# Optimization experiments

Measured on AMD Instinct MI355X. Metric: run time of the kernel, lower is better.

## Reference

```python
import jax, jax.numpy as jnp
import numpy as np

N_STREAMS = 8
DIM = 1024
N_HEADS = 16
HEAD_DIM = DIM // N_HEADS
STREAM_DIM = DIM // N_STREAMS
EPS = 1e-6


def setup_inputs() -> dict:
    key = jax.random.key(0)
    ks = jax.random.split(key, 20)
    B, S, D = 2, 2048, DIM
    inp = {
        "x": jax.random.normal(ks[0], (B, S, D), jnp.float32),
        "rope_cos": jax.random.uniform(ks[1], (S, HEAD_DIM), jnp.float32),
        "rope_sin": jax.random.uniform(ks[2], (S, HEAD_DIM), jnp.float32),
        # DeltaOperator: learned per-channel decay logits
        "delta_decay": jax.random.normal(ks[3], (D,), jnp.float32) * 0.02,
        # gate_proj: Linear(D, 3*n)
        "gate_w": jax.random.normal(ks[4], (3 * N_STREAMS, D), jnp.float32) * 0.02,
        "gate_b": jnp.zeros((3 * N_STREAMS,), jnp.float32),
        "phi_res": jax.random.normal(ks[5], (N_STREAMS, N_STREAMS), jnp.float32) * 0.02,
        "ln1_w": jnp.ones((D,), jnp.float32),
        "ln2_w": jnp.ones((D,), jnp.float32),
        # MLP (StrategicLinear == Linear at inference)
        "w1": jax.random.normal(ks[6], (4 * D, D), jnp.float32) * 0.02,
        "b1": jnp.zeros((4 * D,), jnp.float32),
        "w2": jax.random.normal(ks[7], (D, 4 * D), jnp.float32) * 0.02,
        "b2": jnp.zeros((D,), jnp.float32),
        # nn.MultiheadAttention params
        "in_proj_w": jax.random.normal(ks[8], (3 * D, D), jnp.float32) * 0.02,
        "in_proj_b": jnp.zeros((3 * D,), jnp.float32),
        "out_w": jax.random.normal(ks[9], (D, D), jnp.float32) * 0.02,
        "out_b": jnp.zeros((D,), jnp.float32),
    }
    return inp


def delta_operator(x, decay_logits):
    # out_t = x_t - s_{t-1};  s_t = beta*s_{t-1} + (1-beta)*x_t  (per-channel EMA delta)
    beta = jax.nn.sigmoid(decay_logits)  # [D]

    def step(s, xt):
        out = xt - s
        s_new = beta * s + (1.0 - beta) * xt
        return s_new, out

    xT = jnp.swapaxes(x, 0, 1)  # [S,B,D]
    s0 = jnp.zeros_like(xT[0])
    _, ysT = jax.lax.scan(step, s0, xT)
    return jnp.swapaxes(ysT, 0, 1)  # [B,S,D]


def rms_norm(x, w):
    var = jnp.mean(x * x, axis=-1, keepdims=True)
    return x * jax.lax.rsqrt(var + EPS) * w


def sinkhorn_knopp(phi, iterations=15):
    K = jnp.exp(phi)
    for _ in range(iterations):
        K = K / jnp.sum(K, axis=1, keepdims=True)
        K = K / jnp.sum(K, axis=0, keepdims=True)
    return K


def causal_mha(x, in_proj_w, in_proj_b, out_w, out_b):
    B, S, D = x.shape
    qkv = x @ in_proj_w.T + in_proj_b  # [B,S,3D]
    q, k, v = jnp.split(qkv, 3, axis=-1)
    def heads(t):
        return t.reshape(B, S, N_HEADS, HEAD_DIM).transpose(0, 2, 1, 3)  # [B,H,S,hd]
    q, k, v = heads(q), heads(k), heads(v)
    scores = jnp.einsum("bhqd,bhkd->bhqk", q, k) / jnp.sqrt(jnp.float32(HEAD_DIM))
    mask = jnp.tril(jnp.ones((S, S), bool))
    scores = jnp.where(mask, scores, jnp.float32(-1e9))
    attn = jax.nn.softmax(scores, axis=-1)
    o = jnp.einsum("bhqk,bhkd->bhqd", attn, v)
    o = o.transpose(0, 2, 1, 3).reshape(B, S, D)
    return o @ out_w.T + out_b


def reference(x, rope_cos, rope_sin, delta_decay, gate_w, gate_b, phi_res,
              ln1_w, ln2_w, w1, b1, w2, b2, in_proj_w, in_proj_b, out_w, out_b):
    B, S, D = x.shape
    n = N_STREAMS
    x_delta = delta_operator(x, delta_decay)
    x_state = jnp.mean(x_delta, axis=1)  # [B,D]
    gates = x_state @ gate_w.T + gate_b  # [B,3n]
    g_res = jax.nn.sigmoid(gates[:, 2 * n:])[:, None, :, None]  # [B,1,n,1]
    H_res = sinkhorn_knopp(phi_res, 15)
    x_streams = x_delta.reshape(B, S, n, STREAM_DIM)
    # (x_perm @ H.T).permute back == einsum over stream axis
    mhc_out = jnp.einsum("bsnd,mn->bsmd", x_streams * g_res, H_res).reshape(B, S, D)
    normed = rms_norm(x_delta, ln1_w)
    attn_out = causal_mha(normed, in_proj_w, in_proj_b, out_w, out_b)
    normed2 = rms_norm(x_delta + attn_out, ln2_w)
    h = jax.nn.gelu(normed2 @ w1.T + b1, approximate=False)
    ffn_out = h @ w2.T + b2
    return x_delta + attn_out + ffn_out + mhc_out
```

## Files before the change

### kernel.cpp

```cpp
#include <hip/hip_runtime.h>
#include <hip/hip_bf16.h>
#include <math.h>

#define BB 2
#define SS 2048
#define DDIM 1024
#define NHEAD 16
#define NSTR 8
#define SDIMC 128
#define NCH 16
#define CLEN 128
#define EPSV 1e-6f

using bf16 = __hip_bfloat16;
typedef __attribute__((ext_vector_type(8))) __bf16 bf8;
typedef __attribute__((ext_vector_type(4))) __bf16 bf4v;
typedef __attribute__((ext_vector_type(4))) float f4;

__device__ __forceinline__ bf16 f2b(float v) { return __float2bfloat16(v); }
__device__ __forceinline__ bf8 ld8(const bf16* p) { return *(const bf8*)p; }
__device__ __forceinline__ f4 MFMA(bf8 a, bf8 b, f4 c) {
  return __builtin_amdgcn_mfma_f32_16x16x32_bf16(a, b, c, 0, 0, 0);
}
__device__ __forceinline__ float sigm(float x) { return 1.0f / (1.0f + expf(-x)); }
__device__ __forceinline__ float fexp2(float x) { return __builtin_amdgcn_exp2f(x); }

__device__ __forceinline__ float gelu_f(float v) {
  float x = v * 0.70710678118654752f;
  float ax = fabsf(x);
  float t = __builtin_amdgcn_rcpf(1.0f + 0.3275911f * ax);
  float p = ((((1.061405429f * t - 1.453152027f) * t + 1.421413741f) * t
              - 0.284496736f) * t + 0.254829592f) * t;
  float e = 1.0f - p * fexp2(-ax * ax * 1.4426950408889634f);
  e = copysignf(e, x);
  return 0.5f * v * (1.0f + e);
}

__device__ __forceinline__ void glds16(bf16* l, const bf16* g) {
  __builtin_amdgcn_global_load_lds(
      (const __attribute__((address_space(1))) unsigned int*)g,
      (__attribute__((address_space(3))) unsigned int*)l, 16, 0, 0);
}

__global__ __launch_bounds__(256) void cvt_all(const float* __restrict__ ipw,
                                               const float* __restrict__ ow,
                                               const float* __restrict__ w1,
                                               const float* __restrict__ w2,
                                               bf16* __restrict__ WIPW,
                                               bf16* __restrict__ WOW,
                                               bf16* __restrict__ W1B,
                                               bf16* __restrict__ W2B) {
  const int S1 = 3 * DDIM * DDIM, S2 = S1 + DDIM * DDIM,
            S3 = S2 + 4 * DDIM * DDIM;
  int i4 = (blockIdx.x * 256 + threadIdx.x) * 4;
  const float* src;
  bf16* dst;
  int off;
  if (i4 < S1)      { src = ipw; dst = WIPW; off = i4; }
  else if (i4 < S2) { src = ow;  dst = WOW;  off = i4 - S1; }
  else if (i4 < S3) { src = w1;  dst = W1B;  off = i4 - S2; }
  else              { src = w2;  dst = W2B;  off = i4 - S3; }
  float4 v = *(const float4*)(src + off);
  bf4v o;
  o[0] = (__bf16)v.x; o[1] = (__bf16)v.y; o[2] = (__bf16)v.z; o[3] = (__bf16)v.w;
  *(bf4v*)(dst + off) = o;
}

__global__ __launch_bounds__(256) void delta_passA(const float* __restrict__ x,
                                                   const float* __restrict__ decay,
                                                   float* __restrict__ SA) {
  int idx = blockIdx.x * 256 + threadIdx.x;
  int d = idx % DDIM;
  int c = (idx / DDIM) % NCH;
  int b = idx / (DDIM * NCH);
  float beta = sigm(decay[d]);
  float omb = 1.0f - beta;
  const float* xp = x + ((size_t)(b * SS + c * CLEN)) * DDIM + d;
  float s = 0.0f;
  for (int j = 0; j < CLEN; j++) {
    float xv = xp[(size_t)j * DDIM];
    s = beta * s + omb * xv;
  }
  SA[idx] = s;
}

__global__ __launch_bounds__(256) void delta_passB(const float* __restrict__ SA,
                                                   const float* __restrict__ decay,
                                                   float* __restrict__ SIN) {
  int idx = blockIdx.x * 256 + threadIdx.x;
  int d = idx % DDIM;
  int b = idx / DDIM;
  float beta = sigm(decay[d]);
  float p = beta;
  for (int i = 0; i < 7; i++) p *= p;
  float s = 0.0f;
  for (int c = 0; c < NCH; c++) {
    SIN[(b * NCH + c) * DDIM + d] = s;
    s = p * s + SA[(b * NCH + c) * DDIM + d];
  }
}

__global__ __launch_bounds__(256) void delta_passC(const float* __restrict__ x,
                                                   const float* __restrict__ decay,
                                                   const float* __restrict__ SIN,
                                                   float* __restrict__ XD,
                                                   float* __restrict__ SA) {
  int idx = blockIdx.x * 256 + threadIdx.x;
  int d = idx % DDIM;
  int c = (idx / DDIM) % NCH;
  int b = idx / (DDIM * NCH);
  float beta = sigm(decay[d]);
  float omb = 1.0f - beta;
  const float* xp = x + ((size_t)(b * SS + c * CLEN)) * DDIM + d;
  float* xdp = XD + ((size_t)(b * SS + c * CLEN)) * DDIM + d;
  float s = SIN[idx];
  float sum = 0.0f;
  for (int j = 0; j < CLEN; j++) {
    float xv = xp[(size_t)j * DDIM];
    float o = xv - s;
    xdp[(size_t)j * DDIM] = o;
    sum += o;
    s = beta * s + omb * xv;
  }
  SA[idx] = sum;
}

__global__ __launch_bounds__(1024) void gates_sinkhorn(const float* __restrict__ SA,
                                                       const float* __restrict__ gw,
                                                       const float* __restrict__ gb,
                                                       const float* __restrict__ phi,
                                                       float* __restrict__ gres,
                                                       float* __restrict__ hres) {
  int tid = threadIdx.x;
  int wave = tid >> 6, lane = tid & 63;
  int b = wave >> 3, j = wave & 7;
  float acc = 0.0f;
  for (int d = lane; d < DDIM; d += 64) {
    float xs = 0.0f;
    for (int c = 0; c < NCH; c++) xs += SA[(b * NCH + c) * DDIM + d];
    xs *= (1.0f / (float)SS);
    acc += xs * gw[(2 * NSTR + j) * DDIM + d];
  }
  for (int off = 32; off > 0; off >>= 1) acc += __shfl_down(acc, off);
  if (lane == 0) gres[b * NSTR + j] = sigm(acc + gb[2 * NSTR + j]);
  __syncthreads();
  if (tid == 0) {
    float Km[8][8];
    for (int i = 0; i < 8; i++)
      for (int jj = 0; jj < 8; jj++) Km[i][jj] = expf(phi[i * 8 + jj]);
    for (int it = 0; it < 15; it++) {
      for (int i = 0; i < 8; i++) {
        float rs = 0.0f;
        for (int jj = 0; jj < 8; jj++) rs += Km[i][jj];
        float inv = 1.0f / rs;
        for (int jj = 0; jj < 8; jj++) Km[i][jj] *= inv;
      }
      for (int jj = 0; jj < 8; jj++) {
        float cs = 0.0f;
        for (int i = 0; i < 8; i++) cs += Km[i][jj];
        float inv = 1.0f / cs;
        for (int i = 0; i < 8; i++) Km[i][jj] *= inv;
      }
    }
    for (int i = 0; i < 8; i++)
      for (int jj = 0; jj < 8; jj++) hres[i * 8 + jj] = Km[i][jj];
  }
}

__global__ __launch_bounds__(256) void rmsnorm_k(const float* __restrict__ in,
                                                 const float* __restrict__ w,
                                                 bf16* __restrict__ out) {
  int row = blockIdx.x;
  const float* r = in + (size_t)row * DDIM;
  int tid = threadIdx.x;
  float ss = 0.0f;
  for (int i = tid; i < DDIM; i += 256) {
    float v = r[i];
    ss += v * v;
  }
  for (int off = 32; off > 0; off >>= 1) ss += __shfl_down(ss, off);
  __shared__ float red[4];
  if ((tid & 63) == 0) red[tid >> 6] = ss;
  __syncthreads();
  float tot = red[0] + red[1] + red[2] + red[3];
  float sc = rsqrtf(tot / (float)DDIM + EPSV);
  bf16* o = out + (size_t)row * DDIM;
  for (int i = tid; i < DDIM; i += 256) o[i] = f2b(r[i] * sc * w[i]);
}

template <int ODT, int EPI>
__global__ __launch_bounds__(256) void gemm_lds(const bf16* __restrict__ A,
                                                const bf16* __restrict__ W,
                                                const float* __restrict__ bias,
                                                const float* __restrict__ res,
                                                void* __restrict__ outp,
                                                int M, int N, int K) {
  __shared__ bf16 As[2][128 * 32];
  __shared__ bf16 Bs[2][128 * 32];
  int tid = threadIdx.x;
  int lane = tid & 63, wv = tid >> 6;
  int ml = lane & 15, quad = lane >> 4;
  int wr = wv >> 1, wc = wv & 1;
  int m0 = blockIdx.x * 128, n0 = blockIdx.y * 128;
  const bf16* ga[2];
  const bf16* gb[2];
  int lofs[2];
#pragma unroll
  for (int it = 0; it < 2; it++) {
    int c = it * 256 + tid;
    int row = c >> 2, kc = (c & 3) * 8;
    ga[it] = A + (size_t)(m0 + row) * K + kc;
    gb[it] = W + (size_t)(n0 + row) * K + kc;
    lofs[it] = c * 8;
  }
#pragma unroll
  for (int it = 0; it < 2; it++) {
    glds16(&As[0][lofs[it]], ga[it]);
    glds16(&Bs[0][lofs[it]], gb[it]);
  }
  f4 acc[4][4] = {};
  int nk = K >> 5;
  int cur = 0;
  __syncthreads();
  for (int t = 0; t < nk; t++) {
    if (t + 1 < nk) {
      int ko = (t + 1) * 32;
#pragma unroll
      for (int it = 0; it < 2; it++) {
        glds16(&As[cur ^ 1][lofs[it]], ga[it] + ko);
        glds16(&Bs[cur ^ 1][lofs[it]], gb[it] + ko);
      }
    }
    bf8 af[4], bfr[4];
#pragma unroll
    for (int mi = 0; mi < 4; mi++)
      af[mi] = ld8(&As[cur][(wr * 64 + mi * 16 + ml) * 32 + quad * 8]);
#pragma unroll
    for (int ni = 0; ni < 4; ni++)
      bfr[ni] = ld8(&Bs[cur][(wc * 64 + ni * 16 + ml) * 32 + quad * 8]);
#pragma unroll
    for (int mi = 0; mi < 4; mi++)
#pragma unroll
      for (int ni = 0; ni < 4; ni++)
        acc[mi][ni] = MFMA(af[mi], bfr[ni], acc[mi][ni]);
    __syncthreads();
    cur ^= 1;
  }
#pragma unroll
  for (int mi = 0; mi < 4; mi++)
#pragma unroll
    for (int ni = 0; ni < 4; ni++)
#pragma unroll
      for (int r = 0; r < 4; r++) {
        int row = m0 + wr * 64 + mi * 16 + quad * 4 + r;
        int col = n0 + wc * 64 + ni * 16 + ml;
        size_t idx = (size_t)row * N + col;
        float v = acc[mi][ni][r] + bias[col];
        if (EPI == 1) v = gelu_f(v);
        if (EPI == 2) v += res[idx];
        if (ODT == 1) ((bf16*)outp)[idx] = f2b(v);
        else ((float*)outp)[idx] = v;
      }
}

__global__ __launch_bounds__(256) void gemm_part2(const bf16* __restrict__ A,
                                                  const bf16* __restrict__ W,
                                                  float* __restrict__ P0,
                                                  float* __restrict__ P1,
                                                  int M, int N, int KS, int LDK) {
  __shared__ bf16 As[2][128 * 32];
  __shared__ bf16 Bs[2][128 * 32];
  int tid = threadIdx.x;
  int lane = tid & 63, wv = tid >> 6;
  int ml = lane & 15, quad = lane >> 4;
  int wr = wv >> 1, wc = wv & 1;
  int m0 = blockIdx.x * 128, n0 = blockIdx.y * 128;
  const bf16* Ab = A + blockIdx.z * KS;
  const bf16* Wb = W + blockIdx.z * KS;
  float* P = blockIdx.z ? P1 : P0;
  const bf16* ga[2];
  const bf16* gb[2];
  int lofs[2];
#pragma unroll
  for (int it = 0; it < 2; it++) {
    int c = it * 256 + tid;
    int row = c >> 2, kc = (c & 3) * 8;
    ga[it] = Ab + (size_t)(m0 + row) * LDK + kc;
    gb[it] = Wb + (size_t)(n0 + row) * LDK + kc;
    lofs[it] = c * 8;
  }
#pragma unroll
  for (int it = 0; it < 2; it++) {
    glds16(&As[0][lofs[it]], ga[it]);
    glds16(&Bs[0][lofs[it]], gb[it]);
  }
  f4 acc[4][4] = {};
  int nk = KS >> 5;
  int cur = 0;
  __syncthreads();
  for (int t = 0; t < nk; t++) {
    if (t + 1 < nk) {
      int ko = (t + 1) * 32;
#pragma unroll
      for (int it = 0; it < 2; it++) {
        glds16(&As[cur ^ 1][lofs[it]], ga[it] + ko);
        glds16(&Bs[cur ^ 1][lofs[it]], gb[it] + ko);
      }
    }
    bf8 af[4], bfr[4];
#pragma unroll
    for (int mi = 0; mi < 4; mi++)
      af[mi] = ld8(&As[cur][(wr * 64 + mi * 16 + ml) * 32 + quad * 8]);
#pragma unroll
    for (int ni = 0; ni < 4; ni++)
      bfr[ni] = ld8(&Bs[cur][(wc * 64 + ni * 16 + ml) * 32 + quad * 8]);
#pragma unroll
    for (int mi = 0; mi < 4; mi++)
#pragma unroll
      for (int ni = 0; ni < 4; ni++)
        acc[mi][ni] = MFMA(af[mi], bfr[ni], acc[mi][ni]);
    __syncthreads();
    cur ^= 1;
  }
#pragma unroll
  for (int mi = 0; mi < 4; mi++)
#pragma unroll
    for (int ni = 0; ni < 4; ni++)
#pragma unroll
      for (int r = 0; r < 4; r++) {
        int row = m0 + wr * 64 + mi * 16 + quad * 4 + r;
        int col = n0 + wc * 64 + ni * 16 + ml;
        P[(size_t)row * N + col] = acc[mi][ni][r];
      }
}

template <int ODT, int EPI>
__global__ __launch_bounds__(256) void gemm_lds64(const bf16* __restrict__ A,
                                                  const bf16* __restrict__ W,
                                                  const float* __restrict__ bias,
                                                  const float* __restrict__ res,
                                                  void* __restrict__ outp,
                                                  int M, int N, int K) {
  __shared__ bf16 As[2][64 * 32];
  __shared__ bf16 Bs[2][128 * 32];
  int tid = threadIdx.x;
  int lane = tid & 63, wv = tid >> 6;
  int ml = lane & 15, quad = lane >> 4;
  int wr = wv & 1, wc = wv >> 1;
  int m0 = blockIdx.x * 64, n0 = blockIdx.y * 128;
  const bf16* gaA;
  const bf16* gb[2];
  int lofA, lofs[2];
  {
    int c = tid;
    int row = c >> 2, kc = (c & 3) * 8;
    gaA = A + (size_t)(m0 + row) * K + kc;
    lofA = c * 8;
  }
#pragma unroll
  for (int it = 0; it < 2; it++) {
    int c = it * 256 + tid;
    int row = c >> 2, kc = (c & 3) * 8;
    gb[it] = W + (size_t)(n0 + row) * K + kc;
    lofs[it] = c * 8;
  }
  glds16(&As[0][lofA], gaA);
#pragma unroll
  for (int it = 0; it < 2; it++) glds16(&Bs[0][lofs[it]], gb[it]);
  f4 acc[2][4] = {};
  int nk = K >> 5;
  int cur = 0;
  __syncthreads();
  for (int t = 0; t < nk; t++) {
    if (t + 1 < nk) {
      int ko = (t + 1) * 32;
      glds16(&As[cur ^ 1][lofA], gaA + ko);
#pragma unroll
      for (int it = 0; it < 2; it++) glds16(&Bs[cur ^ 1][lofs[it]], gb[it] + ko);
    }
    bf8 af[2], bfr[4];
#pragma unroll
    for (int mi = 0; mi < 2; mi++)
      af[mi] = ld8(&As[cur][(wr * 32 + mi * 16 + ml) * 32 + quad * 8]);
#pragma unroll
    for (int ni = 0; ni < 4; ni++)
      bfr[ni] = ld8(&Bs[cur][(wc * 64 + ni * 16 + ml) * 32 + quad * 8]);
#pragma unroll
    for (int mi = 0; mi < 2; mi++)
#pragma unroll
      for (int ni = 0; ni < 4; ni++)
        acc[mi][ni] = MFMA(af[mi], bfr[ni], acc[mi][ni]);
    __syncthreads();
    cur ^= 1;
  }
#pragma unroll
  for (int mi = 0; mi < 2; mi++)
#pragma unroll
    for (int ni = 0; ni < 4; ni++)
#pragma unroll
      for (int r = 0; r < 4; r++) {
        int row = m0 + wr * 32 + mi * 16 + quad * 4 + r;
        int col = n0 + wc * 64 + ni * 16 + ml;
        size_t idx = (size_t)row * N + col;
        float v = acc[mi][ni][r] + bias[col];
        if (EPI == 1) v = gelu_f(v);
        if (EPI == 2) v += res[idx];
        if (ODT == 1) ((bf16*)outp)[idx] = f2b(v);
        else ((float*)outp)[idx] = v;
      }
}

__global__ __launch_bounds__(256) void vtrans(const bf16* __restrict__ qkv,
                                              bf16* __restrict__ VT) {
  int bid = blockIdx.x;
  int st = bid % (SS / 64);
  int h = (bid / (SS / 64)) % NHEAD;
  int b = bid / ((SS / 64) * NHEAD);
  __shared__ bf16 tile[64][65];
  int s0 = st * 64;
  int tid = threadIdx.x;
  for (int it = 0; it < 16; it++) {
    int sl = it * 4 + (tid >> 6), dl = tid & 63;
    tile[sl][dl] = qkv[(size_t)(b * SS + s0 + sl) * (3 * DDIM) + 2 * DDIM + h * 64 + dl];
  }
  __syncthreads();
  for (int it = 0; it < 16; it++) {
    int dl = it * 4 + (tid >> 6), sl = tid & 63;
    VT[((size_t)(b * NHEAD + h) * 64 + dl) * SS + s0 + sl] = tile[sl][dl];
  }
}

__device__ __forceinline__ void phase_tile(int kt, int q0, int nkt,
                                           const bf8* qf, f4* oacc,
                                           float* m_r, float* l_r,
                                           const bf16* __restrict__ Ks,
                                           const bf16* __restrict__ Vs,
                                           bf16 (*pl)[72], int ml, int quad) {
  if (kt >= nkt) return;
  const float SC = 0.125f * 1.44269504089f;
  int k0 = kt * 64;
  f4 sacc[4] = {{0,0,0,0},{0,0,0,0},{0,0,0,0},{0,0,0,0}};
  __builtin_amdgcn_s_setprio(1);
#pragma unroll
  for (int kk = 0; kk < 2; kk++)
#pragma unroll
    for (int c = 0; c < 4; c++) {
      int chunk = ((c * 16 + ml) << 3) + ((kk * 4 + quad) ^ (ml & 7));
      bf8 kf = ld8(&Ks[chunk * 8]);
      sacc[c] = MFMA(qf[kk], kf, sacc[c]);
    }
  __builtin_amdgcn_s_setprio(0);
  float sv[4][4];
#pragma unroll
  for (int c = 0; c < 4; c++)
#pragma unroll
    for (int r = 0; r < 4; r++) sv[c][r] = sacc[c][r] * SC;
  if (kt == nkt - 1) {
#pragma unroll
    for (int c = 0; c < 4; c++)
#pragma unroll
      for (int r = 0; r < 4; r++) {
        int qi = q0 + quad * 4 + r;
        int kj = k0 + c * 16 + ml;
        if (kj > qi) sv[c][r] = -1e9f;
      }
  }
  float alpha[4];
#pragma unroll
  for (int r = 0; r < 4; r++) {
    float mx = fmaxf(fmaxf(sv[0][r], sv[1][r]), fmaxf(sv[2][r], sv[3][r]));
#pragma unroll
    for (int off = 1; off < 16; off <<= 1) mx = fmaxf(mx, __shfl_xor(mx, off));
    float mn = fmaxf(m_r[r], mx);
    float rs = 0.0f;
#pragma unroll
    for (int c = 0; c < 4; c++) {
      float p = fexp2(sv[c][r] - mn);
      sv[c][r] = p;
      rs += p;
    }
#pragma unroll
    for (int off = 1; off < 16; off <<= 1) rs += __shfl_xor(rs, off);
    alpha[r] = fexp2(m_r[r] - mn);
    l_r[r] = l_r[r] * alpha[r] + rs;
    m_r[r] = mn;
  }
#pragma unroll
  for (int c = 0; c < 4; c++)
#pragma unroll
    for (int r = 0; r < 4; r++) oacc[c][r] *= alpha[r];
#pragma unroll
  for (int c = 0; c < 4; c++)
#pragma unroll
    for (int r = 0; r < 4; r++)
      pl[quad * 4 + r][c * 16 + ml] = f2b(sv[c][r]);
  bf8 pf[2];
#pragma unroll
  for (int kk = 0; kk < 2; kk++) pf[kk] = ld8(&pl[ml][kk * 32 + quad * 8]);
  __builtin_amdgcn_s_setprio(1);
#pragma unroll
  for (int c = 0; c < 4; c++)
#pragma unroll
    for (int kk = 0; kk < 2; kk++) {
      int chunk = ((c * 16 + ml) << 3) + ((kk * 4 + quad) ^ (ml & 7));
      bf8 vf = ld8(&Vs[chunk * 8]);
      oacc[c] = MFMA(pf[kk], vf, oacc[c]);
    }
  __builtin_amdgcn_s_setprio(0);
}

__global__ __launch_bounds__(256) void flash_attn(const bf16* __restrict__ qkv,
                                                  const bf16* __restrict__ VT,
                                                  bf16* __restrict__ obuf) {
  int rb = blockIdx.x;
  int bid = (rb & 7) * 64 + (rb >> 3);
  int j = bid & 15;
  int blk = (j & 1) ? (15 - (j >> 1)) : (j >> 1);
  int h = (bid >> 4) & 15;
  int b = bid >> 8;
  int tid = threadIdx.x;
  int wv = tid >> 6, lane = tid & 63;
  int ml = lane & 15, quad = lane >> 4;
  int idx0 = blk * 4 + wv;
  int idx1 = 127 - idx0;
  int q0a = idx0 * 16, q0b = idx1 * 16;
  int nkt0 = blk + 1;
  int nkt1 = 32 - blk;
  int maxn = nkt1;

  __shared__ __align__(16) bf16 Ks[2][64 * 64];
  __shared__ __align__(16) bf16 Vs[2][64 * 64];
  __shared__ __align__(16) bf16 plds[4][16][72];
  bf16 (*pl)[72] = plds[wv];

  bf8 qfa[2], qfb[2];
#pragma unroll
  for (int kk = 0; kk < 2; kk++) {
    qfa[kk] = ld8(qkv + (size_t)(b * SS + q0a + ml) * (3 * DDIM) + h * 64 + kk * 32 + quad * 8);
    qfb[kk] = ld8(qkv + (size_t)(b * SS + q0b + ml) * (3 * DDIM) + h * 64 + kk * 32 + quad * 8);
  }
  f4 oacca[4] = {{0,0,0,0},{0,0,0,0},{0,0,0,0},{0,0,0,0}};
  f4 oaccb[4] = {{0,0,0,0},{0,0,0,0},{0,0,0,0},{0,0,0,0}};
  float ma[4], la[4], mb[4], lb[4];
#pragma unroll
  for (int r = 0; r < 4; r++) {
    ma[r] = -1e30f; la[r] = 0.0f;
    mb[r] = -1e30f; lb[r] = 0.0f;
  }

  const bf16* kglob = qkv + (size_t)b * SS * (3 * DDIM) + DDIM + h * 64;
  const bf16* vglob = VT + (size_t)(b * NHEAD + h) * 64 * SS;

#pragma unroll
  for (int it = 0; it < 2; it++) {
    int lam = it * 256 + tid;
    int row = lam >> 3;
    int ch = (lam & 7) ^ (row & 7);
    glds16(&Ks[0][lam * 8], kglob + (size_t)row * (3 * DDIM) + ch * 8);
    glds16(&Vs[0][lam * 8], vglob + (size_t)row * SS + ch * 8);
  }
  __syncthreads();
  int cur = 0;
  for (int kt = 0; kt < maxn; kt++) {
    if (kt + 1 < maxn) {
      int k0n = (kt + 1) * 64;
#pragma unroll
      for (int it = 0; it < 2; it++) {
        int lam = it * 256 + tid;
        int row = lam >> 3;
        int ch = (lam & 7) ^ (row & 7);
        glds16(&Ks[cur ^ 1][lam * 8], kglob + (size_t)(k0n + row) * (3 * DDIM) + ch * 8);
        glds16(&Vs[cur ^ 1][lam * 8], vglob + (size_t)row * SS + k0n + ch * 8);
      }
    }
    phase_tile(kt, q0a, nkt0, qfa, oacca, ma, la, Ks[cur], Vs[cur], pl, ml, quad);
    phase_tile(kt, q0b, nkt1, qfb, oaccb, mb, lb, Ks[cur], Vs[cur], pl, ml, quad);
    __syncthreads();
    cur ^= 1;
  }
#pragma unroll
  for (int c = 0; c < 4; c++)
#pragma unroll
    for (int r = 0; r < 4; r++) {
      int rowa = q0a + quad * 4 + r;
      int rowb = q0b + quad * 4 + r;
      obuf[(size_t)(b * SS + rowa) * DDIM + h * 64 + c * 16 + ml] =
          f2b(oacca[c][r] / la[r]);
      obuf[(size_t)(b * SS + rowb) * DDIM + h * 64 + c * 16 + ml] =
          f2b(oaccb[c][r] / lb[r]);
    }
}

__global__ __launch_bounds__(256) void final_k(const float* __restrict__ y,
                                               const float* __restrict__ P0,
                                               const float* __restrict__ P1,
                                               const float* __restrict__ bias,
                                               const float* __restrict__ xd,
                                               const float* __restrict__ hres,
                                               const float* __restrict__ gres,
                                               float* __restrict__ out) {
  int row = blockIdx.x;
  int b = row / SS;
  int tid = threadIdx.x;
  __shared__ float cf[8][8];
  if (tid < 64) cf[tid >> 3][tid & 7] = hres[tid] * gres[b * NSTR + (tid & 7)];
  __syncthreads();
  const float* yr = y + (size_t)row * DDIM;
  const float* p0 = P0 + (size_t)row * DDIM;
  const float* p1 = P1 + (size_t)row * DDIM;
  const float* xr = xd + (size_t)row * DDIM;
  float* o = out + (size_t)row * DDIM;
  for (int i = tid; i < DDIM; i += 256) {
    int m = i >> 7, dd = i & 127;
    float acc = yr[i] + p0[i] + p1[i] + bias[i];
#pragma unroll
    for (int n = 0; n < 8; n++) acc += cf[m][n] * xr[n * SDIMC + dd];
    o[i] = acc;
  }
}

extern "C" void kernel_launch(void* const* d_in, const int* in_sizes, int n_in,
                              void* d_out, int out_size, void* d_ws, size_t ws_size,
                              hipStream_t stream) {
  const float* x     = (const float*)d_in[0];
  const float* decay = (const float*)d_in[3];
  const float* gw    = (const float*)d_in[4];
  const float* gb    = (const float*)d_in[5];
  const float* phi   = (const float*)d_in[6];
  const float* ln1   = (const float*)d_in[7];
  const float* ln2   = (const float*)d_in[8];
  const float* w1    = (const float*)d_in[9];
  const float* b1    = (const float*)d_in[10];
  const float* w2    = (const float*)d_in[11];
  const float* b2    = (const float*)d_in[12];
  const float* ipw   = (const float*)d_in[13];
  const float* ipb   = (const float*)d_in[14];
  const float* ow    = (const float*)d_in[15];
  const float* obs   = (const float*)d_in[16];
  float* out = (float*)d_out;

  const size_t MB = 1048576ull;
  char* wsp = (char*)d_ws;
  float* SA   = (float*)(wsp);
  float* SIN  = (float*)(wsp + 131072ull);
  float* GRES = (float*)(wsp + 262144ull);
  float* HRES = (float*)(wsp + 262208ull);
  float* XD   = (float*)(wsp + 1 * MB);
  float* AO   = (float*)(wsp + 17 * MB);
  bf16*  NORM = (bf16*)(wsp + 33 * MB);
  bf16*  OB   = (bf16*)(wsp + 41 * MB);
  bf16*  QKV  = (bf16*)(wsp + 49 * MB);
  bf16*  VT   = (bf16*)(wsp + 73 * MB);
  bf16*  HB   = (bf16*)(wsp + 49 * MB);
  bf16*  WIPW = (bf16*)(wsp + 81 * MB);
  bf16*  WOW  = (bf16*)(wsp + 87 * MB);
  bf16*  W1B  = (bf16*)(wsp + 89 * MB);
  bf16*  W2B  = (bf16*)(wsp + 97 * MB);
  float* PK0  = (float*)(wsp + 33 * MB);
  float* PK1  = (float*)(wsp + 81 * MB);

  cvt_all<<<dim3(12 * DDIM * DDIM / 1024), dim3(256), 0, stream>>>(
      ipw, ow, w1, w2, WIPW, WOW, W1B, W2B);

  delta_passA<<<dim3(BB * NCH * DDIM / 256), dim3(256), 0, stream>>>(x, decay, SA);
  delta_passB<<<dim3(BB * DDIM / 256), dim3(256), 0, stream>>>(SA, decay, SIN);
  delta_passC<<<dim3(BB * NCH * DDIM / 256), dim3(256), 0, stream>>>(x, decay, SIN, XD, SA);
  gates_sinkhorn<<<dim3(1), dim3(1024), 0, stream>>>(SA, gw, gb, phi, GRES, HRES);
  rmsnorm_k<<<dim3(BB * SS), dim3(256), 0, stream>>>(XD, ln1, NORM);
  gemm_lds<1, 0><<<dim3(32, 24), dim3(256), 0, stream>>>(NORM, WIPW, ipb, nullptr,
                                                         QKV, BB * SS, 3 * DDIM, DDIM);
  vtrans<<<dim3(BB * NHEAD * (SS / 64)), dim3(256), 0, stream>>>(QKV, VT);
  flash_attn<<<dim3(BB * NHEAD * 16), dim3(256), 0, stream>>>(QKV, VT, OB);
  gemm_lds64<0, 2><<<dim3(64, 8), dim3(256), 0, stream>>>(OB, WOW, obs, XD,
                                                          AO, BB * SS, DDIM, DDIM);
  rmsnorm_k<<<dim3(BB * SS), dim3(256), 0, stream>>>(AO, ln2, NORM);
  gemm_lds<1, 1><<<dim3(32, 32), dim3(256), 0, stream>>>(NORM, W1B, b1, nullptr,
                                                         HB, BB * SS, 4 * DDIM, DDIM);
  gemm_part2<<<dim3(32, 8, 2), dim3(256), 0, stream>>>(HB, W2B, PK0, PK1,
                                                       BB * SS, DDIM, 2 * DDIM, 4 * DDIM);
  final_k<<<dim3(BB * SS), dim3(256), 0, stream>>>(AO, PK0, PK1, b2, XD,
                                                   HRES, GRES, out);
}
```

Measured before the change: 443.6 us.

## Share K/V register fragments across both query tiles and transpose QK scores

The flash attention loop now loads K and V fragments from LDS into registers once per key tile and reuses them for both the short and long query tiles, where before each tile reloaded them. The QK MFMA operands are swapped so each lane holds the scores for one query row. That lets the row max and row sum use two cross-lane shuffles instead of four per row, and lets P be written to LDS as packed 4-wide stores. Per-wave P staging is split into two buffers so the two tiles' softmax and PV phases can be interleaved, at the cost of more registers and LDS.

New measurement: 425.6 us. 4.0% less time.

```diff
diff --git a/kernel.cpp b/kernel.cpp
--- a/kernel.cpp
+++ b/kernel.cpp
@@ -430,82 +430,78 @@
   }
 }
 
-__device__ __forceinline__ void phase_tile(int kt, int q0, int nkt,
-                                           const bf8* qf, f4* oacc,
-                                           float* m_r, float* l_r,
-                                           const bf16* __restrict__ Ks,
-                                           const bf16* __restrict__ Vs,
-                                           bf16 (*pl)[72], int ml, int quad) {
-  if (kt >= nkt) return;
+__device__ __forceinline__ void qk_softmax(bool active, int kt, int q0, int nkt,
+                                           const bf8 kf[4][2], const bf8* qf,
+                                           f4* oacc, float& m, float& l,
+                                           bf8* pf, bf16 (*pl)[72],
+                                           int ml, int quad, int k0) {
+  if (!active) return;
   const float SC = 0.125f * 1.44269504089f;
-  int k0 = kt * 64;
-  f4 sacc[4] = {{0,0,0,0},{0,0,0,0},{0,0,0,0},{0,0,0,0}};
+  f4 s[4] = {{0,0,0,0},{0,0,0,0},{0,0,0,0},{0,0,0,0}};
   __builtin_amdgcn_s_setprio(1);
 #pragma unroll
   for (int kk = 0; kk < 2; kk++)
 #pragma unroll
-    for (int c = 0; c < 4; c++) {
-      int chunk = ((c * 16 + ml) << 3) + ((kk * 4 + quad) ^ (ml & 7));
-      bf8 kf = ld8(&Ks[chunk * 8]);
-      sacc[c] = MFMA(qf[kk], kf, sacc[c]);
+    for (int c = 0; c < 4; c++)
+      s[c] = MFMA(kf[c][kk], qf[kk], s[c]);
+  __builtin_amdgcn_s_setprio(0);
+  if (kt == nkt - 1) {
+    int qi = q0 + ml;
+#pragma unroll
+    for (int c = 0; c < 4; c++)
+#pragma unroll
+      for (int r = 0; r < 4; r++)
+        if (k0 + c * 16 + quad * 4 + r > qi) s[c][r] = -1e30f;
+  }
+  float mx = s[0][0];
+#pragma unroll
+  for (int c = 0; c < 4; c++)
+#pragma unroll
+    for (int r = 0; r < 4; r++) mx = fmaxf(mx, s[c][r]);
+  mx = fmaxf(mx, __shfl_xor(mx, 16));
+  mx = fmaxf(mx, __shfl_xor(mx, 32));
+  float mn = fmaxf(m, mx * SC);
+  float alpha = fexp2(m - mn);
+  float rs = 0.0f;
+  float p[4][4];
+#pragma unroll
+  for (int c = 0; c < 4; c++)
+#pragma unroll
+    for (int r = 0; r < 4; r++) {
+      p[c][r] = fexp2(__builtin_fmaf(s[c][r], SC, -mn));
+      rs += p[c][r];
     }
-  __builtin_amdgcn_s_setprio(0);
-  float sv[4][4];
+  rs += __shfl_xor(rs, 16);
+  rs += __shfl_xor(rs, 32);
+  l = l * alpha + rs;
+  m = mn;
+  float alr[4];
+#pragma unroll
+  for (int r = 0; r < 4; r++) alr[r] = __shfl(alpha, quad * 4 + r);
 #pragma unroll
   for (int c = 0; c < 4; c++)
 #pragma unroll
-    for (int r = 0; r < 4; r++) sv[c][r] = sacc[c][r] * SC;
-  if (kt == nkt - 1) {
-#pragma unroll
-    for (int c = 0; c < 4; c++)
-#pragma unroll
-      for (int r = 0; r < 4; r++) {
-        int qi = q0 + quad * 4 + r;
-        int kj = k0 + c * 16 + ml;
-        if (kj > qi) sv[c][r] = -1e9f;
-      }
-  }
-  float alpha[4];
-#pragma unroll
-  for (int r = 0; r < 4; r++) {
-    float mx = fmaxf(fmaxf(sv[0][r], sv[1][r]), fmaxf(sv[2][r], sv[3][r]));
-#pragma unroll
-    for (int off = 1; off < 16; off <<= 1) mx = fmaxf(mx, __shfl_xor(mx, off));
-    float mn = fmaxf(m_r[r], mx);
-    float rs = 0.0f;
-#pragma unroll
-    for (int c = 0; c < 4; c++) {
-      float p = fexp2(sv[c][r] - mn);
-      sv[c][r] = p;
-      rs += p;
-    }
-#pragma unroll
-    for (int off = 1; off < 16; off <<= 1) rs += __shfl_xor(rs, off);
-    alpha[r] = fexp2(m_r[r] - mn);
-    l_r[r] = l_r[r] * alpha[r] + rs;
-    m_r[r] = mn;
-  }
+    for (int r = 0; r < 4; r++) oacc[c][r] *= alr[r];
+#pragma unroll
+  for (int c = 0; c < 4; c++) {
+    bf4v w;
+#pragma unroll
+    for (int r = 0; r < 4; r++) w[r] = (__bf16)p[c][r];
+    *(bf4v*)&pl[ml][c * 16 + quad * 4] = w;
+  }
+#pragma unroll
+  for (int kk = 0; kk < 2; kk++) pf[kk] = ld8(&pl[ml][kk * 32 + quad * 8]);
+}
+
+__device__ __forceinline__ void pv_acc(bool active, const bf8* pf,
+                                       const bf8 vf[4][2], f4* oacc) {
+  if (!active) return;
+  __builtin_amdgcn_s_setprio(1);
 #pragma unroll
   for (int c = 0; c < 4; c++)
 #pragma unroll
-    for (int r = 0; r < 4; r++) oacc[c][r] *= alpha[r];
-#pragma unroll
-  for (int c = 0; c < 4; c++)
-#pragma unroll
-    for (int r = 0; r < 4; r++)
-      pl[quad * 4 + r][c * 16 + ml] = f2b(sv[c][r]);
-  bf8 pf[2];
-#pragma unroll
-  for (int kk = 0; kk < 2; kk++) pf[kk] = ld8(&pl[ml][kk * 32 + quad * 8]);
-  __builtin_amdgcn_s_setprio(1);
-#pragma unroll
-  for (int c = 0; c < 4; c++)
-#pragma unroll
-    for (int kk = 0; kk < 2; kk++) {
-      int chunk = ((c * 16 + ml) << 3) + ((kk * 4 + quad) ^ (ml & 7));
-      bf8 vf = ld8(&Vs[chunk * 8]);
-      oacc[c] = MFMA(pf[kk], vf, oacc[c]);
-    }
+    for (int kk = 0; kk < 2; kk++)
+      oacc[c] = MFMA(pf[kk], vf[c][kk], oacc[c]);
   __builtin_amdgcn_s_setprio(0);
 }
 
@@ -530,8 +526,9 @@
 
   __shared__ __align__(16) bf16 Ks[2][64 * 64];
   __shared__ __align__(16) bf16 Vs[2][64 * 64];
-  __shared__ __align__(16) bf16 plds[4][16][72];
-  bf16 (*pl)[72] = plds[wv];
+  __shared__ __align__(16) bf16 plds[4][2][16][72];
+  bf16 (*plA)[72] = plds[wv][0];
+  bf16 (*plB)[72] = plds[wv][1];
 
   bf8 qfa[2], qfb[2];
 #pragma unroll
@@ -541,12 +538,7 @@
   }
   f4 oacca[4] = {{0,0,0,0},{0,0,0,0},{0,0,0,0},{0,0,0,0}};
   f4 oaccb[4] = {{0,0,0,0},{0,0,0,0},{0,0,0,0},{0,0,0,0}};
-  float ma[4], la[4], mb[4], lb[4];
-#pragma unroll
-  for (int r = 0; r < 4; r++) {
-    ma[r] = -1e30f; la[r] = 0.0f;
-    mb[r] = -1e30f; lb[r] = 0.0f;
-  }
+  float ma = -1e30f, la = 0.0f, mb = -1e30f, lb = 0.0f;
 
   const bf16* kglob = qkv + (size_t)b * SS * (3 * DDIM) + DDIM + h * 64;
   const bf16* vglob = VT + (size_t)(b * NHEAD + h) * 64 * SS;
@@ -562,6 +554,7 @@
   __syncthreads();
   int cur = 0;
   for (int kt = 0; kt < maxn; kt++) {
+    int k0 = kt * 64;
     if (kt + 1 < maxn) {
       int k0n = (kt + 1) * 64;
 #pragma unroll
@@ -573,10 +566,36 @@
         glds16(&Vs[cur ^ 1][lam * 8], vglob + (size_t)row * SS + k0n + ch * 8);
       }
     }
-    phase_tile(kt, q0a, nkt0, qfa, oacca, ma, la, Ks[cur], Vs[cur], pl, ml, quad);
-    phase_tile(kt, q0b, nkt1, qfb, oaccb, mb, lb, Ks[cur], Vs[cur], pl, ml, quad);
+    bool act0 = kt < nkt0;
+    bf8 kf[4][2];
+#pragma unroll
+    for (int kk = 0; kk < 2; kk++)
+#pragma unroll
+      for (int c = 0; c < 4; c++) {
+        int chunk = ((c * 16 + ml) << 3) + ((kk * 4 + quad) ^ (ml & 7));
+        kf[c][kk] = ld8(&Ks[cur][chunk * 8]);
+      }
+    bf8 pfa[2], pfb[2];
+    qk_softmax(act0, kt, q0a, nkt0, kf, qfa, oacca, ma, la, pfa, plA, ml, quad, k0);
+    qk_softmax(true, kt, q0b, nkt1, kf, qfb, oaccb, mb, lb, pfb, plB, ml, quad, k0);
+    bf8 vf[4][2];
+#pragma unroll
+    for (int kk = 0; kk < 2; kk++)
+#pragma unroll
+      for (int c = 0; c < 4; c++) {
+        int chunk = ((c * 16 + ml) << 3) + ((kk * 4 + quad) ^ (ml & 7));
+        vf[c][kk] = ld8(&Vs[cur][chunk * 8]);
+      }
+    pv_acc(act0, pfa, vf, oacca);
+    pv_acc(true, pfb, vf, oaccb);
     __syncthreads();
     cur ^= 1;
+  }
+  float lna[4], lnb[4];
+#pragma unroll
+  for (int r = 0; r < 4; r++) {
+    lna[r] = __shfl(la, quad * 4 + r);
+    lnb[r] = __shfl(lb, quad * 4 + r);
   }
 #pragma unroll
   for (int c = 0; c < 4; c++)
@@ -585,9 +604,9 @@
       int rowa = q0a + quad * 4 + r;
       int rowb = q0b + quad * 4 + r;
       obuf[(size_t)(b * SS + rowa) * DDIM + h * 64 + c * 16 + ml] =
-          f2b(oacca[c][r] / la[r]);
+          f2b(oacca[c][r] / lna[r]);
       obuf[(size_t)(b * SS + rowb) * DDIM + h * 64 + c * 16 + ml] =
-          f2b(oaccb[c][r] / lb[r]);
+          f2b(oaccb[c][r] / lnb[r]);
     }
 }
 
```
